# Kernel optimization log

Measured on AMD Instinct MI355X. Metric: run time of the kernel, lower is better.

The kernel has to match this reference:

```python
import jax, jax.numpy as jnp
import numpy as np

SHIFT_SIZE = 5
PAD = SHIFT_SIZE // 2  # 2


def _shift_list(pad, C):
    # matches CycleFC.shiftlist: [-p..p] + [p-1..-(p-1)] tiled to length C
    base = list(range(-pad, pad + 1)) + list(range(pad - 1, -pad, -1))
    n = C // len(base) + 1
    return (base * n)[:C]


def cycle_shift_vertical(x, pad):
    # x: (B, C, H, W). Per-channel shift along H with zero fill.
    # Equivalent to pad+per-channel roll+crop in the torch code (|shift| <= pad).
    B, C, H, W = x.shape
    shifts = jnp.array(_shift_list(pad, C))                     # (C,)
    padded = jnp.pad(x, ((0, 0), (0, 0), (pad, pad), (0, 0)))    # (B,C,H+2p,W)
    row_idx = pad + jnp.arange(H)[None, :] - shifts[:, None]     # (C,H), in [0, H+2p)
    return jnp.take_along_axis(padded, row_idx[None, :, :, None], axis=2)  # (B,C,H,W)


def setup_inputs() -> dict:
    key = jax.random.key(0)
    ks = jax.random.split(key, 11)
    B, H, W, C = 16, 56, 56, 384
    Cq = C // 4
    s = lambda k, shp, fan: jax.random.normal(k, shp, jnp.float32) * (1.0 / np.sqrt(fan))
    return {
        "x": jax.random.normal(ks[0], (B, H, W, C), jnp.float32),
        "w_h": s(ks[1], (C, C), C), "b_h": jnp.zeros((C,), jnp.float32),
        "w_c": s(ks[2], (C, C), C), "b_c": jnp.zeros((C,), jnp.float32),
        "w_r1": s(ks[3], (C, Cq), C), "b_r1": jnp.zeros((Cq,), jnp.float32),
        "w_r2": s(ks[4], (Cq, 3 * C), Cq), "b_r2": jnp.zeros((3 * C,), jnp.float32),
        "w_p": s(ks[5], (C, C), C), "b_p": jnp.zeros((C,), jnp.float32),
    }


def reference(x, w_h, b_h, w_c, b_c, w_r1, b_r1, w_r2, b_r2, w_p, b_p):
    B, H, W, C = x.shape
    # vertical per-channel cyclic shift (NB: original forward uses vertical_shift
    # and proj_h for BOTH branches, so x_w == x_h; reproduced faithfully)
    xs = cycle_shift_vertical(jnp.transpose(x, (0, 3, 1, 2)), PAD)  # (B,C,H,W)
    xs = jnp.transpose(xs, (0, 2, 3, 1))                             # (B,H,W,C)
    x_h = xs @ w_h + b_h
    x_w = x_h
    x_c = x @ w_c + b_c
    # channel reweighting
    a = jnp.mean(x_h + x_w + x_c, axis=(1, 2))                       # (B,C)
    a = jax.nn.gelu(a @ w_r1 + b_r1, approximate=False) @ w_r2 + b_r2  # (B,3C)
    a = a.reshape(B, C, 3).transpose(2, 0, 1)                        # (3,B,C)
    a = jax.nn.softmax(a, axis=0)[:, :, None, None, :]               # (3,B,1,1,C)
    out = x_h * a[0] + x_w * a[1] + x_c * a[2]
    return out @ w_p + b_p
```

## Files before the change

kernel.cpp:

```cpp
#include <hip/hip_runtime.h>
#include <hip/hip_bf16.h>

#define HH 56
#define WWD 56
#define CC 384
#define HWW (HH*WWD)
#define MM (16*HWW)
#define MBPB 49
#define NBLK3 (16*MBPB)
#define WB_BSTRIDE (24*24576)

typedef __attribute__((ext_vector_type(8))) short bf16x8;
typedef __attribute__((ext_vector_type(4))) int   int4v;
typedef __attribute__((ext_vector_type(4))) float f32x4;

__device__ __forceinline__ unsigned short f2bf(float f) {
    union { float f; unsigned u; } v; v.f = f;
    unsigned r = v.u + 0x7fffu + ((v.u >> 16) & 1u);
    return (unsigned short)(r >> 16);
}
__device__ __forceinline__ float bf2f(unsigned short h) {
    union { unsigned u; float f; } v; v.u = ((unsigned)h) << 16;
    return v.f;
}
__device__ __forceinline__ bf16x8 asbf(int4v v) {
    union { int4v i; bf16x8 b; } u; u.i = v; return u.b;
}

__device__ __forceinline__ int invp(int k) {
    if (k < 48)  return 8*k;
    if (k < 144) { int j = k-48;  return 8*(j>>1) + ((j&1) ? 7 : 1); }
    if (k < 240) { int j = k-144; return 8*(j>>1) + ((j&1) ? 6 : 2); }
    if (k < 336) { int j = k-240; return 8*(j>>1) + ((j&1) ? 5 : 3); }
    return 8*(k-336) + 4;
}
__device__ __forceinline__ int fwdp(int c) {
    int q = c >> 3, s = c & 7;
    switch (s) {
        case 0: return q;
        case 1: return 48 + 2*q;
        case 7: return 49 + 2*q;
        case 2: return 144 + 2*q;
        case 6: return 145 + 2*q;
        case 3: return 240 + 2*q;
        case 5: return 241 + 2*q;
        default: return 336 + q;
    }
}
__device__ __forceinline__ int dcls(int k) {
    return k < 48 ? 2 : k < 144 ? 1 : k < 240 ? 0 : k < 336 ? -1 : -2;
}

__global__ __launch_bounds__(384)
void prep_x(const float* __restrict__ x, unsigned short* __restrict__ xt,
            float* __restrict__ R)
{
    __shared__ float buf[4][CC];
    int bid = blockIdx.x;
    int b = bid / HH, h = bid - b*HH;
    int t = threadIdx.x;
    int wsub = t / 96, q = t - wsub*96;
    int kd0 = fwdp(4*q), kd1 = fwdp(4*q+1), kd2 = fwdp(4*q+2), kd3 = fwdp(4*q+3);
    const float* xp = x + ((size_t)bid*WWD)*CC;
    unsigned short* xo = xt + ((size_t)b*HWW + h)*CC + t;
    float rs = 0.f;
    for (int w0 = 0; w0 < WWD; w0 += 4) {
        float4 v = *(const float4*)(xp + (size_t)(w0 + wsub)*CC + 4*q);
        buf[wsub][kd0] = v.x; buf[wsub][kd1] = v.y;
        buf[wsub][kd2] = v.z; buf[wsub][kd3] = v.w;
        __syncthreads();
        #pragma unroll
        for (int i = 0; i < 4; ++i) {
            float fv = buf[i][t];
            rs += fv;
            xo[(size_t)(w0 + i)*HH*CC] = f2bf(fv);
        }
        __syncthreads();
    }
    R[(size_t)bid*CC + t] = rs;
}

__global__ __launch_bounds__(384)
void mean_k(const float* __restrict__ R,
            float* __restrict__ mhp, float* __restrict__ mcp)
{
    int b = blockIdx.x, t = threadIdx.x;
    const float* Rb = R + (size_t)b*HH*CC;
    float S = 0.f;
    #pragma unroll 8
    for (int h = 0; h < HH; ++h) S += Rb[(size_t)h*CC + t];
    int d = dcls(t);
    float adj = 0.f;
    if (d == 2)       adj = Rb[0*CC + t] + Rb[1*CC + t];
    else if (d == 1)  adj = Rb[0*CC + t];
    else if (d == -1) adj = Rb[55*CC + t];
    else if (d == -2) adj = Rb[54*CC + t] + Rb[55*CC + t];
    const float inv = 1.f / (float)HWW;
    int c = invp(t);
    mhp[(size_t)b*CC + c] = (S - adj) * inv;
    mcp[(size_t)b*CC + c] = S * inv;
}

__global__ __launch_bounds__(384)
void avec_k(const float* __restrict__ mhp, const float* __restrict__ mcp,
            const float* __restrict__ w_h, const float* __restrict__ w_c,
            float2* __restrict__ part)
{
    __shared__ float sm[2][96];
    int p = blockIdx.x, b = blockIdx.y, t = threadIdx.x;
    if (t < 96)       sm[0][t]     = mhp[(size_t)b*CC + 96*p + t];
    else if (t < 192) sm[1][t-96]  = mcp[(size_t)b*CC + 96*p + (t-96)];
    __syncthreads();
    const float* ph = w_h + (size_t)(96*p)*CC + t;
    const float* pc = w_c + (size_t)(96*p)*CC + t;
    float sh = 0.f, sc = 0.f;
    #pragma unroll 8
    for (int e = 0; e < 96; ++e) {
        sh += sm[0][e] * ph[(size_t)e*CC];
        sc += sm[1][e] * pc[(size_t)e*CC];
    }
    part[((size_t)b*4 + p)*CC + t] = make_float2(sh, sc);
}

__global__ __launch_bounds__(384)
void lam_fin(const float2* __restrict__ part,
             const float* __restrict__ b_h, const float* __restrict__ b_c,
             const float* __restrict__ w_r1, const float* __restrict__ b_r1,
             const float* __restrict__ w_r2, const float* __restrict__ b_r2,
             float2* __restrict__ lam, float* __restrict__ biasc)
{
    __shared__ float aa[CC], r1p[4][96];
    int b = blockIdx.x, t = threadIdx.x;
    float2 p0 = part[((size_t)b*4 + 0)*CC + t];
    float2 p1 = part[((size_t)b*4 + 1)*CC + t];
    float2 p2 = part[((size_t)b*4 + 2)*CC + t];
    float2 p3 = part[((size_t)b*4 + 3)*CC + t];
    float sh = p0.x + p1.x + p2.x + p3.x;
    float sc = p0.y + p1.y + p2.y + p3.y;
    aa[t] = 2.f*(sh + b_h[t]) + (sc + b_c[t]);
    __syncthreads();
    {
        int j = t % 96, p = t / 96;
        float s = 0.f;
        #pragma unroll 8
        for (int k = p*96; k < p*96 + 96; ++k) s += aa[k] * w_r1[(size_t)k*96 + j];
        r1p[p][j] = s;
    }
    __syncthreads();
    if (t < 96) {
        float s = r1p[0][t] + r1p[1][t] + r1p[2][t] + r1p[3][t] + b_r1[t];
        r1p[0][t] = 0.5f*s*(1.f + erff(s*0.70710678118654752f));
    }
    __syncthreads();
    float s0 = b_r2[3*t], s1 = b_r2[3*t+1], s2 = b_r2[3*t+2];
    #pragma unroll 8
    for (int q = 0; q < 96; ++q) {
        float rv = r1p[0][q];
        const float* wp = w_r2 + (size_t)q*(3*CC) + 3*t;
        s0 += rv*wp[0]; s1 += rv*wp[1]; s2 += rv*wp[2];
    }
    float mx = fmaxf(s0, fmaxf(s1, s2));
    float e0 = expf(s0-mx), e1 = expf(s1-mx), e2 = expf(s2-mx);
    float dn = 1.f/(e0+e1+e2);
    float lh = (e0+e1)*dn, lc = e2*dn;
    lam[(size_t)b*CC + t] = make_float2(lh, lc);
    biasc[(size_t)b*CC + t] = lh*b_h[t] + lc*b_c[t];
}

__global__ __launch_bounds__(256)
void prepP_k(const float* __restrict__ w_p, char* __restrict__ wP3)
{
    int j = blockIdx.x*256 + threadIdx.x;
    int kt = j / 1536, f = j - kt*1536;
    int wnx = f / 384, r = f - wnx*384;
    int ni = r / 64, lane = r - ni*64;
    int n = wnx*96 + ni*16 + (lane & 15);
    int k0 = kt*32 + ((lane >> 4) << 3);
    bf16x8 o;
    #pragma unroll
    for (int e = 0; e < 8; ++e) o[e] = (short)f2bf(w_p[(size_t)(k0 + e)*CC + n]);
    *(bf16x8*)(wP3 + (size_t)kt*24576 + wnx*6144 + ni*1024 + lane*16) = o;
}

__global__ __launch_bounds__(512, 2)
void wfold_k(const float* __restrict__ w_h, const float* __restrict__ w_c,
             const float2* __restrict__ lam, const char* __restrict__ wP3,
             unsigned short* __restrict__ Wf)
{
    __shared__ char Asm[96*768];
    const int tid = threadIdx.x;
    const int kq = blockIdx.x, which = blockIdx.y, b = blockIdx.z;

    const int lane = tid & 63;
    const int wid  = tid >> 6;
    const int l16  = lane & 15;
    const int lhi  = lane >> 4;
    const int wm  = (wid >> 2) * 48;
    const int wnx = wid & 3;
    const int wn  = wnx * 96;

    const char* bptr = wP3 + wnx*6144 + lane*16;
    const float* wsrc = which ? w_c : w_h;

    int4v bb[3][3];
    #pragma unroll
    for (int e = 0; e < 3; ++e) bb[0][e] = *(const int4v*)(bptr + e*1024);
    #pragma unroll
    for (int e = 0; e < 3; ++e) bb[1][e] = *(const int4v*)(bptr + 3072 + e*1024);

    #pragma unroll
    for (int it = 0; it < 9; ++it) {
        int s = it*512 + tid;
        if (s < 96*48) {
            int rr = s / 48, oct = s - rr*48;
            int c = invp(kq*96 + rr);
            const float* src = wsrc + (size_t)c*CC + oct*8;
            const float2* lp = lam + (size_t)b*CC + oct*8;
            bf16x8 o;
            #pragma unroll
            for (int e = 0; e < 8; ++e) {
                float2 L = lp[e];
                float s_ = which ? L.y : L.x;
                o[e] = (short)f2bf(src[e] * s_);
            }
            *(bf16x8*)(Asm + rr*768 + ((oct ^ (rr & 7)) << 4)) = o;
        }
    }

    f32x4 acc[3][6];
    #pragma unroll
    for (int mi = 0; mi < 3; ++mi)
        #pragma unroll
        for (int ni = 0; ni < 6; ++ni) acc[mi][ni] = (f32x4)0.f;

    int4v a[3];
    __syncthreads();

    #pragma unroll
    for (int v = 0; v < 24; ++v) {
        if (v + 2 < 24) {
            const int vn = v + 2, vt = vn >> 1;
            const char* nb = bptr + (size_t)vt*24576 + (vn & 1)*3072;
            #pragma unroll
            for (int e = 0; e < 3; ++e)
                bb[vn % 3][e] = *(const int4v*)(nb + e*1024);
        }
        if ((v & 1) == 0) {
            const int kt = v >> 1;
            const int octg = kt*4 + lhi;
            #pragma unroll
            for (int mi = 0; mi < 3; ++mi) {
                int r = wm + mi*16 + l16;
                a[mi] = *(const int4v*)(Asm + r*768 + ((octg ^ (r & 7)) << 4));
            }
        }
        #pragma unroll
        for (int mi = 0; mi < 3; ++mi)
            #pragma unroll
            for (int e = 0; e < 3; ++e)
                acc[mi][(v & 1)*3 + e] = __builtin_amdgcn_mfma_f32_16x16x32_bf16(
                    asbf(a[mi]), asbf(bb[v % 3][e]), acc[mi][(v & 1)*3 + e], 0, 0, 0);
    }

    unsigned short* wout = Wf + ((size_t)(b*2 + which)*CC)*CC;
    #pragma unroll
    for (int ni = 0; ni < 6; ++ni) {
        int p = wn + ni*16 + l16;
        #pragma unroll
        for (int mi = 0; mi < 3; ++mi) {
            int row0 = kq*96 + wm + mi*16 + lhi*4;
            #pragma unroll
            for (int j = 0; j < 4; ++j)
                wout[(size_t)(row0 + j)*CC + p] = f2bf(acc[mi][ni][j]);
        }
    }
}

__global__ __launch_bounds__(256)
void repack_k(const unsigned short* __restrict__ Wf, char* __restrict__ wB3)
{
    int idx = blockIdx.x*256 + threadIdx.x;
    int b = idx / (24*1536);
    int rem = idx - b*(24*1536);
    int kt = rem / 1536, f = rem - kt*1536;
    int wnx = f / 384, r = f - wnx*384;
    int ni = r / 64, lane = r - ni*64;
    int p = wnx*96 + ni*16 + (lane & 15);
    int k0 = kt*32 + ((lane >> 4) << 3);
    int hp = k0 >= 384;
    int kk = k0 - (hp ? 384 : 0);
    const unsigned short* src = Wf + ((size_t)(b*2 + hp)*CC + kk)*CC + p;
    bf16x8 o;
    #pragma unroll
    for (int e = 0; e < 8; ++e) o[e] = (short)src[(size_t)e*CC];
    *(bf16x8*)(wB3 + (size_t)b*WB_BSTRIDE + (size_t)kt*24576 + wnx*6144 + ni*1024 + lane*16) = o;
}

__global__ __launch_bounds__(384)
void bvec_k(const float* __restrict__ v, const float* __restrict__ w_p,
            float* __restrict__ part2)
{
    __shared__ float sm[96];
    int p4 = blockIdx.x, b = blockIdx.y, t = threadIdx.x;
    if (t < 96) sm[t] = v[(size_t)b*CC + 96*p4 + t];
    __syncthreads();
    const float* pp = w_p + (size_t)(96*p4)*CC + t;
    float s = 0.f;
    #pragma unroll 8
    for (int e = 0; e < 96; ++e) s += sm[e] * pp[(size_t)e*CC];
    part2[((size_t)b*4 + p4)*CC + t] = s;
}

__global__ __launch_bounds__(512, 4)
void gmain(const unsigned short* __restrict__ xt,
           const char* __restrict__ wB3,
           const float* __restrict__ part2,
           const float* __restrict__ b_p,
           float* __restrict__ out)
{
    __shared__ char Asm[68*768];

    const int tid = threadIdx.x;
    int bid = blockIdx.x;
    bid = (bid & 7)*(NBLK3/8) + (bid >> 3);
    const int b  = bid / MBPB;
    const int m0 = (bid - b*MBPB) * 64;
    const size_t gbase = (size_t)b * HWW;

    const int lane = tid & 63;
    const int wid  = tid >> 6;
    const int l16  = lane & 15;
    const int lhi  = lane >> 4;
    const int wm  = (wid >> 2) * 32;
    const int wnx = wid & 3;
    const int wn  = wnx * 96;

    const char* bptr1 = wB3 + (size_t)b*WB_BSTRIDE + wnx*6144 + lane*16;

    int4v bb[3][3];
    #pragma unroll
    for (int e = 0; e < 3; ++e) bb[0][e] = *(const int4v*)(bptr1 + e*1024);
    #pragma unroll
    for (int e = 0; e < 3; ++e) bb[1][e] = *(const int4v*)(bptr1 + 3072 + e*1024);

    #pragma unroll
    for (int it = 0; it < 7; ++it) {
        int s = it*512 + tid;
        if (s < 68*48) {
            int row = s / 48, oct = s - row*48;
            int g = m0 - 2 + row;
            g = g < 0 ? 0 : (g >= HWW ? HWW-1 : g);
            int4v v = __builtin_nontemporal_load(
                (const int4v*)(xt + (gbase + g)*CC + oct*8));
            *(int4v*)(Asm + row*768 + ((oct ^ (row & 7)) << 4)) = v;
        }
    }

    int rbase[2], hmod[2];
    #pragma unroll
    for (int mi = 0; mi < 2; ++mi) {
        rbase[mi] = wm + mi*16 + l16 + 2;
        hmod[mi]  = (m0 + wm + mi*16 + l16) % HH;
    }

    f32x4 acc[2][6];
    #pragma unroll
    for (int mi = 0; mi < 2; ++mi)
        #pragma unroll
        for (int ni = 0; ni < 6; ++ni) acc[mi][ni] = (f32x4)0.f;

    int4v a[2];
    __syncthreads();

    #pragma unroll
    for (int v = 0; v < 48; ++v) {
        if (v + 2 < 48) {
            const int vn = v + 2, vt = vn >> 1;
            const char* nb = bptr1 + (size_t)vt*24576 + (vn & 1)*3072;
            #pragma unroll
            for (int e = 0; e < 3; ++e)
                bb[vn % 3][e] = *(const int4v*)(nb + e*1024);
        }
        if ((v & 1) == 0) {
            const int kt = v >> 1;
            if (kt < 12) {
                const int octg = kt*4 + lhi;
                const int d = octg < 6 ? 2 : octg < 18 ? 1 : octg < 30 ? 0 : octg < 42 ? -1 : -2;
                #pragma unroll
                for (int mi = 0; mi < 2; ++mi) {
                    int r = rbase[mi] + d;
                    int4v av = *(const int4v*)(Asm + r*768 + ((octg ^ (r & 7)) << 4));
                    int ok = ((unsigned)(hmod[mi] + d) < (unsigned)HH) ? ~0 : 0;
                    a[mi] = av & ok;
                }
            } else {
                const int octg = (kt-12)*4 + lhi;
                #pragma unroll
                for (int mi = 0; mi < 2; ++mi) {
                    int r = rbase[mi];
                    a[mi] = *(const int4v*)(Asm + r*768 + ((octg ^ (r & 7)) << 4));
                }
            }
        }
        __builtin_amdgcn_s_setprio(1);
        #pragma unroll
        for (int mi = 0; mi < 2; ++mi)
            #pragma unroll
            for (int e = 0; e < 3; ++e)
                acc[mi][(v & 1)*3 + e] = __builtin_amdgcn_mfma_f32_16x16x32_bf16(
                    asbf(a[mi]), asbf(bb[v % 3][e]), acc[mi][(v & 1)*3 + e], 0, 0, 0);
        __builtin_amdgcn_s_setprio(0);
    }

    #pragma unroll
    for (int ni = 0; ni < 6; ++ni) {
        int n = wn + ni*16 + l16;
        float bias = b_p[n]
                   + part2[((size_t)b*4 + 0)*CC + n]
                   + part2[((size_t)b*4 + 1)*CC + n]
                   + part2[((size_t)b*4 + 2)*CC + n]
                   + part2[((size_t)b*4 + 3)*CC + n];
        #pragma unroll
        for (int mi = 0; mi < 2; ++mi) {
            #pragma unroll
            for (int j = 0; j < 4; ++j) {
                int rl = m0 + wm + mi*16 + lhi*4 + j;
                int hh = rl % HH, ww = rl / HH;
                __builtin_nontemporal_store(acc[mi][ni][j] + bias,
                    out + (gbase + (size_t)(hh*WWD + ww))*CC + n);
            }
        }
    }
}

extern "C" void kernel_launch(void* const* d_in, const int* in_sizes, int n_in,
                              void* d_out, int out_size, void* d_ws, size_t ws_size,
                              hipStream_t stream)
{
    const float* x    = (const float*)d_in[0];
    const float* w_h  = (const float*)d_in[1];
    const float* b_h  = (const float*)d_in[2];
    const float* w_c  = (const float*)d_in[3];
    const float* b_c  = (const float*)d_in[4];
    const float* w_r1 = (const float*)d_in[5];
    const float* b_r1 = (const float*)d_in[6];
    const float* w_r2 = (const float*)d_in[7];
    const float* b_r2 = (const float*)d_in[8];
    const float* w_p  = (const float*)d_in[9];
    const float* b_p  = (const float*)d_in[10];
    float* out = (float*)d_out;

    char* ws = (char*)d_ws;
    unsigned short* xt  = (unsigned short*)(ws);
    char* wB3           = ws + 38535168;
    char* wP3           = ws + 47972352;
    unsigned short* Wf  = (unsigned short*)(ws + 48267264);
    float* R            = (float*)(ws + 57704448);
    float2* lam         = (float2*)(ws + 59080704);
    float* biasc        = (float*)(ws + 59129856);
    float* mhp          = (float*)(ws + 59154432);
    float* mcp          = (float*)(ws + 59179008);
    float2* part        = (float2*)(ws + 59203584);
    float* part2        = (float*)(ws + 59400192);

    prep_x<<<16*HH, 384, 0, stream>>>(x, xt, R);
    mean_k<<<16, 384, 0, stream>>>(R, mhp, mcp);
    avec_k<<<dim3(4, 16), 384, 0, stream>>>(mhp, mcp, w_h, w_c, part);
    lam_fin<<<16, 384, 0, stream>>>(part, b_h, b_c, w_r1, b_r1, w_r2, b_r2, lam, biasc);
    prepP_k<<<(12*1536)/256, 256, 0, stream>>>(w_p, wP3);
    wfold_k<<<dim3(4, 2, 16), 512, 0, stream>>>(w_h, w_c, lam, wP3, Wf);
    repack_k<<<(16*24*1536)/256, 256, 0, stream>>>(Wf, wB3);
    bvec_k<<<dim3(4, 16), 384, 0, stream>>>(biasc, w_p, part2);
    gmain<<<NBLK3, 512, 0, stream>>>(xt, wB3, part2, b_p, out);
}
```

Measured before the change: 135.5 us.

## Fuse small MLP kernels and fold weight repack into wfold via LDS

Merges mean, attention-vector, lambda and output-bias kernels into a single per-batch kernel, and has wfold write its result directly in the MFMA-packed layout through an LDS staging buffer, which removes the separate repack and bias kernels and the Wf round trip through global memory. It also drops the setprio hints and the nontemporal stores in the main GEMM. The cost is a serial 384-long dot product per thread in a 16-block kernel, which has low parallelism, plus extra LDS traffic in wfold.

```diff
diff --git a/kernel.cpp b/kernel.cpp
--- a/kernel.cpp
+++ b/kernel.cpp
@@ -9,6 +9,7 @@
 #define MBPB 49
 #define NBLK3 (16*MBPB)
 #define WB_BSTRIDE (24*24576)
+#define BSTR 772
 
 typedef __attribute__((ext_vector_type(8))) short bf16x8;
 typedef __attribute__((ext_vector_type(4))) int   int4v;
@@ -80,10 +81,31 @@
     R[(size_t)bid*CC + t] = rs;
 }
 
+__global__ __launch_bounds__(256)
+void prepP_k(const float* __restrict__ w_p, char* __restrict__ wP3)
+{
+    int j = blockIdx.x*256 + threadIdx.x;
+    int kt = j / 1536, f = j - kt*1536;
+    int wnx = f / 384, r = f - wnx*384;
+    int ni = r / 64, lane = r - ni*64;
+    int n = wnx*96 + ni*16 + (lane & 15);
+    int k0 = kt*32 + ((lane >> 4) << 3);
+    bf16x8 o;
+    #pragma unroll
+    for (int e = 0; e < 8; ++e) o[e] = (short)f2bf(w_p[(size_t)(k0 + e)*CC + n]);
+    *(bf16x8*)(wP3 + (size_t)kt*24576 + wnx*6144 + ni*1024 + lane*16) = o;
+}
+
 __global__ __launch_bounds__(384)
-void mean_k(const float* __restrict__ R,
-            float* __restrict__ mhp, float* __restrict__ mcp)
-{
+void mlp2(const float* __restrict__ R,
+          const float* __restrict__ w_h, const float* __restrict__ b_h,
+          const float* __restrict__ w_c, const float* __restrict__ b_c,
+          const float* __restrict__ w_r1, const float* __restrict__ b_r1,
+          const float* __restrict__ w_r2, const float* __restrict__ b_r2,
+          const float* __restrict__ w_p, const float* __restrict__ b_p,
+          float2* __restrict__ lam, float* __restrict__ bias2)
+{
+    __shared__ float mh[CC], mc[CC], aa[CC], bc2[CC], r1p[4][96];
     int b = blockIdx.x, t = threadIdx.x;
     const float* Rb = R + (size_t)b*HH*CC;
     float S = 0.f;
@@ -97,46 +119,15 @@
     else if (d == -2) adj = Rb[54*CC + t] + Rb[55*CC + t];
     const float inv = 1.f / (float)HWW;
     int c = invp(t);
-    mhp[(size_t)b*CC + c] = (S - adj) * inv;
-    mcp[(size_t)b*CC + c] = S * inv;
-}
-
-__global__ __launch_bounds__(384)
-void avec_k(const float* __restrict__ mhp, const float* __restrict__ mcp,
-            const float* __restrict__ w_h, const float* __restrict__ w_c,
-            float2* __restrict__ part)
-{
-    __shared__ float sm[2][96];
-    int p = blockIdx.x, b = blockIdx.y, t = threadIdx.x;
-    if (t < 96)       sm[0][t]     = mhp[(size_t)b*CC + 96*p + t];
-    else if (t < 192) sm[1][t-96]  = mcp[(size_t)b*CC + 96*p + (t-96)];
-    __syncthreads();
-    const float* ph = w_h + (size_t)(96*p)*CC + t;
-    const float* pc = w_c + (size_t)(96*p)*CC + t;
+    mh[c] = (S - adj) * inv;
+    mc[c] = S * inv;
+    __syncthreads();
     float sh = 0.f, sc = 0.f;
     #pragma unroll 8
-    for (int e = 0; e < 96; ++e) {
-        sh += sm[0][e] * ph[(size_t)e*CC];
-        sc += sm[1][e] * pc[(size_t)e*CC];
-    }
-    part[((size_t)b*4 + p)*CC + t] = make_float2(sh, sc);
-}
-
-__global__ __launch_bounds__(384)
-void lam_fin(const float2* __restrict__ part,
-             const float* __restrict__ b_h, const float* __restrict__ b_c,
-             const float* __restrict__ w_r1, const float* __restrict__ b_r1,
-             const float* __restrict__ w_r2, const float* __restrict__ b_r2,
-             float2* __restrict__ lam, float* __restrict__ biasc)
-{
-    __shared__ float aa[CC], r1p[4][96];
-    int b = blockIdx.x, t = threadIdx.x;
-    float2 p0 = part[((size_t)b*4 + 0)*CC + t];
-    float2 p1 = part[((size_t)b*4 + 1)*CC + t];
-    float2 p2 = part[((size_t)b*4 + 2)*CC + t];
-    float2 p3 = part[((size_t)b*4 + 3)*CC + t];
-    float sh = p0.x + p1.x + p2.x + p3.x;
-    float sc = p0.y + p1.y + p2.y + p3.y;
+    for (int k = 0; k < CC; ++k) {
+        sh += mh[k] * w_h[(size_t)k*CC + t];
+        sc += mc[k] * w_c[(size_t)k*CC + t];
+    }
     aa[t] = 2.f*(sh + b_h[t]) + (sc + b_c[t]);
     __syncthreads();
     {
@@ -164,30 +155,20 @@
     float dn = 1.f/(e0+e1+e2);
     float lh = (e0+e1)*dn, lc = e2*dn;
     lam[(size_t)b*CC + t] = make_float2(lh, lc);
-    biasc[(size_t)b*CC + t] = lh*b_h[t] + lc*b_c[t];
-}
-
-__global__ __launch_bounds__(256)
-void prepP_k(const float* __restrict__ w_p, char* __restrict__ wP3)
-{
-    int j = blockIdx.x*256 + threadIdx.x;
-    int kt = j / 1536, f = j - kt*1536;
-    int wnx = f / 384, r = f - wnx*384;
-    int ni = r / 64, lane = r - ni*64;
-    int n = wnx*96 + ni*16 + (lane & 15);
-    int k0 = kt*32 + ((lane >> 4) << 3);
-    bf16x8 o;
-    #pragma unroll
-    for (int e = 0; e < 8; ++e) o[e] = (short)f2bf(w_p[(size_t)(k0 + e)*CC + n]);
-    *(bf16x8*)(wP3 + (size_t)kt*24576 + wnx*6144 + ni*1024 + lane*16) = o;
+    bc2[t] = lh*b_h[t] + lc*b_c[t];
+    __syncthreads();
+    float s = b_p[t];
+    #pragma unroll 8
+    for (int n = 0; n < CC; ++n) s += bc2[n] * w_p[(size_t)n*CC + t];
+    bias2[(size_t)b*CC + t] = s;
 }
 
 __global__ __launch_bounds__(512, 2)
 void wfold_k(const float* __restrict__ w_h, const float* __restrict__ w_c,
              const float2* __restrict__ lam, const char* __restrict__ wP3,
-             unsigned short* __restrict__ Wf)
-{
-    __shared__ char Asm[96*768];
+             char* __restrict__ wB3)
+{
+    __shared__ char Asm[96*BSTR];
     const int tid = threadIdx.x;
     const int kq = blockIdx.x, which = blockIdx.y, b = blockIdx.z;
 
@@ -262,60 +243,46 @@
                     asbf(a[mi]), asbf(bb[v % 3][e]), acc[mi][(v & 1)*3 + e], 0, 0, 0);
     }
 
-    unsigned short* wout = Wf + ((size_t)(b*2 + which)*CC)*CC;
+    __syncthreads();
+
     #pragma unroll
     for (int ni = 0; ni < 6; ++ni) {
         int p = wn + ni*16 + l16;
         #pragma unroll
         for (int mi = 0; mi < 3; ++mi) {
-            int row0 = kq*96 + wm + mi*16 + lhi*4;
+            int row0 = wm + mi*16 + lhi*4;
             #pragma unroll
             for (int j = 0; j < 4; ++j)
-                wout[(size_t)(row0 + j)*CC + p] = f2bf(acc[mi][ni][j]);
-        }
-    }
-}
-
-__global__ __launch_bounds__(256)
-void repack_k(const unsigned short* __restrict__ Wf, char* __restrict__ wB3)
-{
-    int idx = blockIdx.x*256 + threadIdx.x;
-    int b = idx / (24*1536);
-    int rem = idx - b*(24*1536);
-    int kt = rem / 1536, f = rem - kt*1536;
-    int wnx = f / 384, r = f - wnx*384;
-    int ni = r / 64, lane = r - ni*64;
-    int p = wnx*96 + ni*16 + (lane & 15);
-    int k0 = kt*32 + ((lane >> 4) << 3);
-    int hp = k0 >= 384;
-    int kk = k0 - (hp ? 384 : 0);
-    const unsigned short* src = Wf + ((size_t)(b*2 + hp)*CC + kk)*CC + p;
-    bf16x8 o;
-    #pragma unroll
-    for (int e = 0; e < 8; ++e) o[e] = (short)src[(size_t)e*CC];
-    *(bf16x8*)(wB3 + (size_t)b*WB_BSTRIDE + (size_t)kt*24576 + wnx*6144 + ni*1024 + lane*16) = o;
-}
-
-__global__ __launch_bounds__(384)
-void bvec_k(const float* __restrict__ v, const float* __restrict__ w_p,
-            float* __restrict__ part2)
-{
-    __shared__ float sm[96];
-    int p4 = blockIdx.x, b = blockIdx.y, t = threadIdx.x;
-    if (t < 96) sm[t] = v[(size_t)b*CC + 96*p4 + t];
-    __syncthreads();
-    const float* pp = w_p + (size_t)(96*p4)*CC + t;
-    float s = 0.f;
-    #pragma unroll 8
-    for (int e = 0; e < 96; ++e) s += sm[e] * pp[(size_t)e*CC];
-    part2[((size_t)b*4 + p4)*CC + t] = s;
+                *(unsigned short*)(Asm + (row0 + j)*BSTR + p*2) = f2bf(acc[mi][ni][j]);
+        }
+    }
+    __syncthreads();
+
+    #pragma unroll
+    for (int fi = 0; fi < 9; ++fi) {
+        int flat = fi*512 + tid;
+        int lane2 = flat & 63;
+        int t2 = flat >> 6;
+        int ni2 = t2 % 6;
+        int t3 = t2 / 6;
+        int wnx2 = t3 & 3;
+        int skt = t3 >> 2;
+        int p2 = wnx2*96 + ni2*16 + (lane2 & 15);
+        int rl0 = skt*32 + ((lane2 >> 4) << 3);
+        bf16x8 o;
+        #pragma unroll
+        for (int e = 0; e < 8; ++e)
+            o[e] = (short)*(const unsigned short*)(Asm + (rl0 + e)*BSTR + p2*2);
+        int kt_g = which*12 + kq*3 + skt;
+        *(bf16x8*)(wB3 + (size_t)b*WB_BSTRIDE + (size_t)kt_g*24576
+                   + wnx2*6144 + ni2*1024 + lane2*16) = o;
+    }
 }
 
 __global__ __launch_bounds__(512, 4)
 void gmain(const unsigned short* __restrict__ xt,
            const char* __restrict__ wB3,
-           const float* __restrict__ part2,
-           const float* __restrict__ b_p,
+           const float* __restrict__ bias2,
            float* __restrict__ out)
 {
     __shared__ char Asm[68*768];
@@ -402,32 +369,25 @@
                 }
             }
         }
-        __builtin_amdgcn_s_setprio(1);
         #pragma unroll
         for (int mi = 0; mi < 2; ++mi)
             #pragma unroll
             for (int e = 0; e < 3; ++e)
                 acc[mi][(v & 1)*3 + e] = __builtin_amdgcn_mfma_f32_16x16x32_bf16(
                     asbf(a[mi]), asbf(bb[v % 3][e]), acc[mi][(v & 1)*3 + e], 0, 0, 0);
-        __builtin_amdgcn_s_setprio(0);
     }
 
     #pragma unroll
     for (int ni = 0; ni < 6; ++ni) {
         int n = wn + ni*16 + l16;
-        float bias = b_p[n]
-                   + part2[((size_t)b*4 + 0)*CC + n]
-                   + part2[((size_t)b*4 + 1)*CC + n]
-                   + part2[((size_t)b*4 + 2)*CC + n]
-                   + part2[((size_t)b*4 + 3)*CC + n];
+        float bias = bias2[(size_t)b*CC + n];
         #pragma unroll
         for (int mi = 0; mi < 2; ++mi) {
             #pragma unroll
             for (int j = 0; j < 4; ++j) {
                 int rl = m0 + wm + mi*16 + lhi*4 + j;
                 int hh = rl % HH, ww = rl / HH;
-                __builtin_nontemporal_store(acc[mi][ni][j] + bias,
-                    out + (gbase + (size_t)(hh*WWD + ww))*CC + n);
+                out[(gbase + (size_t)(hh*WWD + ww))*CC + n] = acc[mi][ni][j] + bias;
             }
         }
     }
@@ -454,22 +414,14 @@
     unsigned short* xt  = (unsigned short*)(ws);
     char* wB3           = ws + 38535168;
     char* wP3           = ws + 47972352;
-    unsigned short* Wf  = (unsigned short*)(ws + 48267264);
-    float* R            = (float*)(ws + 57704448);
-    float2* lam         = (float2*)(ws + 59080704);
-    float* biasc        = (float*)(ws + 59129856);
-    float* mhp          = (float*)(ws + 59154432);
-    float* mcp          = (float*)(ws + 59179008);
-    float2* part        = (float2*)(ws + 59203584);
-    float* part2        = (float*)(ws + 59400192);
+    float* R            = (float*)(ws + 48267264);
+    float2* lam         = (float2*)(ws + 49643520);
+    float* bias2        = (float*)(ws + 49692672);
 
     prep_x<<<16*HH, 384, 0, stream>>>(x, xt, R);
-    mean_k<<<16, 384, 0, stream>>>(R, mhp, mcp);
-    avec_k<<<dim3(4, 16), 384, 0, stream>>>(mhp, mcp, w_h, w_c, part);
-    lam_fin<<<16, 384, 0, stream>>>(part, b_h, b_c, w_r1, b_r1, w_r2, b_r2, lam, biasc);
     prepP_k<<<(12*1536)/256, 256, 0, stream>>>(w_p, wP3);
-    wfold_k<<<dim3(4, 2, 16), 512, 0, stream>>>(w_h, w_c, lam, wP3, Wf);
-    repack_k<<<(16*24*1536)/256, 256, 0, stream>>>(Wf, wB3);
-    bvec_k<<<dim3(4, 16), 384, 0, stream>>>(biasc, w_p, part2);
-    gmain<<<NBLK3, 512, 0, stream>>>(xt, wB3, part2, b_p, out);
-}
+    mlp2<<<16, 384, 0, stream>>>(R, w_h, b_h, w_c, b_c, w_r1, b_r1,
+                                 w_r2, b_r2, w_p, b_p, lam, bias2);
+    wfold_k<<<dim3(4, 2, 16), 512, 0, stream>>>(w_h, w_c, lam, wP3, wB3);
+    gmain<<<NBLK3, 512, 0, stream>>>(xt, wB3, bias2, out);
+}
```

Result: slower. 159.3 us (+17.5%).

## Fuse weight repack into wfold kernel via shared-memory transpose, split N across blocks

Applied to the files above, without the earlier changes.

The folded-weight kernel now writes its output directly in the MFMA-friendly packed layout expected by the main GEMM, staging results through shared memory instead of writing a row-major intermediate and running a separate repack kernel. The grid is doubled by splitting the output columns into two halves per block, halving per-block accumulator work. This removes one kernel launch and a global round-trip of the intermediate weight matrix. The shared-memory staging and the extra synchronisations add some cost, and the strided 16-bit LDS accesses may cause bank conflicts.

```diff
diff --git a/kernel.cpp b/kernel.cpp
--- a/kernel.cpp
+++ b/kernel.cpp
@@ -9,6 +9,7 @@
 #define MBPB 49
 #define NBLK3 (16*MBPB)
 #define WB_BSTRIDE (24*24576)
+#define BSTR 396
 
 typedef __attribute__((ext_vector_type(8))) short bf16x8;
 typedef __attribute__((ext_vector_type(4))) int   int4v;
@@ -185,28 +186,30 @@
 __global__ __launch_bounds__(512, 2)
 void wfold_k(const float* __restrict__ w_h, const float* __restrict__ w_c,
              const float2* __restrict__ lam, const char* __restrict__ wP3,
-             unsigned short* __restrict__ Wf)
+             char* __restrict__ wB3)
 {
     __shared__ char Asm[96*768];
     const int tid = threadIdx.x;
-    const int kq = blockIdx.x, which = blockIdx.y, b = blockIdx.z;
+    const int kq = blockIdx.x, which = blockIdx.y;
+    const int b = blockIdx.z >> 1, np = blockIdx.z & 1;
 
     const int lane = tid & 63;
     const int wid  = tid >> 6;
     const int l16  = lane & 15;
     const int lhi  = lane >> 4;
-    const int wm  = (wid >> 2) * 48;
-    const int wnx = wid & 3;
-    const int wn  = wnx * 96;
-
-    const char* bptr = wP3 + wnx*6144 + lane*16;
+    const int mg  = wid >> 2;
+    const int nw  = wid & 3;
+    const int panel = np*2 + (nw >> 1);
+    const int sub   = nw & 1;
+
+    const char* bptr = wP3 + panel*6144 + sub*3072 + lane*16;
     const float* wsrc = which ? w_c : w_h;
 
     int4v bb[3][3];
     #pragma unroll
     for (int e = 0; e < 3; ++e) bb[0][e] = *(const int4v*)(bptr + e*1024);
     #pragma unroll
-    for (int e = 0; e < 3; ++e) bb[1][e] = *(const int4v*)(bptr + 3072 + e*1024);
+    for (int e = 0; e < 3; ++e) bb[1][e] = *(const int4v*)(bptr + 24576 + e*1024);
 
     #pragma unroll
     for (int it = 0; it < 9; ++it) {
@@ -227,73 +230,74 @@
         }
     }
 
-    f32x4 acc[3][6];
+    f32x4 acc[3][3];
     #pragma unroll
     for (int mi = 0; mi < 3; ++mi)
         #pragma unroll
-        for (int ni = 0; ni < 6; ++ni) acc[mi][ni] = (f32x4)0.f;
+        for (int e = 0; e < 3; ++e) acc[mi][e] = (f32x4)0.f;
 
     int4v a[3];
     __syncthreads();
 
     #pragma unroll
-    for (int v = 0; v < 24; ++v) {
-        if (v + 2 < 24) {
-            const int vn = v + 2, vt = vn >> 1;
-            const char* nb = bptr + (size_t)vt*24576 + (vn & 1)*3072;
+    for (int kt = 0; kt < 12; ++kt) {
+        if (kt + 2 < 12) {
+            const char* nb = bptr + (size_t)(kt+2)*24576;
             #pragma unroll
             for (int e = 0; e < 3; ++e)
-                bb[vn % 3][e] = *(const int4v*)(nb + e*1024);
-        }
-        if ((v & 1) == 0) {
-            const int kt = v >> 1;
-            const int octg = kt*4 + lhi;
-            #pragma unroll
-            for (int mi = 0; mi < 3; ++mi) {
-                int r = wm + mi*16 + l16;
-                a[mi] = *(const int4v*)(Asm + r*768 + ((octg ^ (r & 7)) << 4));
-            }
+                bb[(kt+2) % 3][e] = *(const int4v*)(nb + e*1024);
+        }
+        const int octg = kt*4 + lhi;
+        #pragma unroll
+        for (int mi = 0; mi < 3; ++mi) {
+            int r = mg*48 + mi*16 + l16;
+            a[mi] = *(const int4v*)(Asm + r*768 + ((octg ^ (r & 7)) << 4));
         }
         #pragma unroll
         for (int mi = 0; mi < 3; ++mi)
             #pragma unroll
             for (int e = 0; e < 3; ++e)
-                acc[mi][(v & 1)*3 + e] = __builtin_amdgcn_mfma_f32_16x16x32_bf16(
-                    asbf(a[mi]), asbf(bb[v % 3][e]), acc[mi][(v & 1)*3 + e], 0, 0, 0);
-    }
-
-    unsigned short* wout = Wf + ((size_t)(b*2 + which)*CC)*CC;
-    #pragma unroll
-    for (int ni = 0; ni < 6; ++ni) {
-        int p = wn + ni*16 + l16;
+                acc[mi][e] = __builtin_amdgcn_mfma_f32_16x16x32_bf16(
+                    asbf(a[mi]), asbf(bb[kt % 3][e]), acc[mi][e], 0, 0, 0);
+    }
+
+    __syncthreads();
+
+    #pragma unroll
+    for (int e = 0; e < 3; ++e) {
+        int pl = (nw >> 1)*96 + sub*48 + e*16 + l16;
         #pragma unroll
         for (int mi = 0; mi < 3; ++mi) {
-            int row0 = kq*96 + wm + mi*16 + lhi*4;
+            int row0 = mg*48 + mi*16 + lhi*4;
             #pragma unroll
             for (int j = 0; j < 4; ++j)
-                wout[(size_t)(row0 + j)*CC + p] = f2bf(acc[mi][ni][j]);
-        }
-    }
-}
-
-__global__ __launch_bounds__(256)
-void repack_k(const unsigned short* __restrict__ Wf, char* __restrict__ wB3)
-{
-    int idx = blockIdx.x*256 + threadIdx.x;
-    int b = idx / (24*1536);
-    int rem = idx - b*(24*1536);
-    int kt = rem / 1536, f = rem - kt*1536;
-    int wnx = f / 384, r = f - wnx*384;
-    int ni = r / 64, lane = r - ni*64;
-    int p = wnx*96 + ni*16 + (lane & 15);
-    int k0 = kt*32 + ((lane >> 4) << 3);
-    int hp = k0 >= 384;
-    int kk = k0 - (hp ? 384 : 0);
-    const unsigned short* src = Wf + ((size_t)(b*2 + hp)*CC + kk)*CC + p;
-    bf16x8 o;
-    #pragma unroll
-    for (int e = 0; e < 8; ++e) o[e] = (short)src[(size_t)e*CC];
-    *(bf16x8*)(wB3 + (size_t)b*WB_BSTRIDE + (size_t)kt*24576 + wnx*6144 + ni*1024 + lane*16) = o;
+                *(unsigned short*)(Asm + (row0 + j)*BSTR + pl*2) = f2bf(acc[mi][e][j]);
+        }
+    }
+    __syncthreads();
+
+    #pragma unroll
+    for (int fi = 0; fi < 5; ++fi) {
+        int flat = fi*512 + tid;
+        if (flat < 2304) {
+            int lane2 = flat & 63;
+            int t2 = flat >> 6;
+            int ni2 = t2 % 6;
+            int t3 = t2 / 6;
+            int ph = t3 & 1;
+            int skt = t3 >> 1;
+            int pl = ph*96 + ni2*16 + (lane2 & 15);
+            int rl0 = skt*32 + ((lane2 >> 4) << 3);
+            bf16x8 o;
+            #pragma unroll
+            for (int e = 0; e < 8; ++e)
+                o[e] = (short)*(const unsigned short*)(Asm + (rl0 + e)*BSTR + pl*2);
+            int wnx2 = np*2 + ph;
+            int kt_g = which*12 + kq*3 + skt;
+            *(bf16x8*)(wB3 + (size_t)b*WB_BSTRIDE + (size_t)kt_g*24576
+                       + wnx2*6144 + ni2*1024 + lane2*16) = o;
+        }
+    }
 }
 
 __global__ __launch_bounds__(384)
@@ -454,22 +458,20 @@
     unsigned short* xt  = (unsigned short*)(ws);
     char* wB3           = ws + 38535168;
     char* wP3           = ws + 47972352;
-    unsigned short* Wf  = (unsigned short*)(ws + 48267264);
-    float* R            = (float*)(ws + 57704448);
-    float2* lam         = (float2*)(ws + 59080704);
-    float* biasc        = (float*)(ws + 59129856);
-    float* mhp          = (float*)(ws + 59154432);
-    float* mcp          = (float*)(ws + 59179008);
-    float2* part        = (float2*)(ws + 59203584);
-    float* part2        = (float*)(ws + 59400192);
+    float* R            = (float*)(ws + 48267264);
+    float2* lam         = (float2*)(ws + 49643520);
+    float* biasc        = (float*)(ws + 49692672);
+    float* mhp          = (float*)(ws + 49717248);
+    float* mcp          = (float*)(ws + 49741824);
+    float2* part        = (float2*)(ws + 49766400);
+    float* part2        = (float*)(ws + 49963008);
 
     prep_x<<<16*HH, 384, 0, stream>>>(x, xt, R);
     mean_k<<<16, 384, 0, stream>>>(R, mhp, mcp);
     avec_k<<<dim3(4, 16), 384, 0, stream>>>(mhp, mcp, w_h, w_c, part);
     lam_fin<<<16, 384, 0, stream>>>(part, b_h, b_c, w_r1, b_r1, w_r2, b_r2, lam, biasc);
     prepP_k<<<(12*1536)/256, 256, 0, stream>>>(w_p, wP3);
-    wfold_k<<<dim3(4, 2, 16), 512, 0, stream>>>(w_h, w_c, lam, wP3, Wf);
-    repack_k<<<(16*24*1536)/256, 256, 0, stream>>>(Wf, wB3);
+    wfold_k<<<dim3(4, 2, 32), 512, 0, stream>>>(w_h, w_c, lam, wP3, wB3);
     bvec_k<<<dim3(4, 16), 384, 0, stream>>>(biasc, w_p, part2);
     gmain<<<NBLK3, 512, 0, stream>>>(xt, wB3, part2, b_p, out);
 }
```

Measured after the change: 124.5 us. 8.1% less time.
